# Performance work log

Hardware: AMD Instinct MI355X
Metric: run time of the kernel (lower is better)

The kernel has to match this reference:

```python
import jax, jax.numpy as jnp
import numpy as np

L_LAYERS = 6
DIM = 256
HEADS = 8
FFN = 1024
EPS_LN = 1e-3  # keras LayerNormalization default epsilon
EPS_ATT = 1e-6


def sine_pos_encoding(seq_len, d):
    pos = jnp.arange(seq_len, dtype=jnp.float32)[:, None]
    i = jnp.arange(d, dtype=jnp.float32)[None, :]
    rate = jnp.power(1e4, -(2.0 * jnp.floor(i / 2.0)) / d)
    ang = pos * rate
    return jnp.where(jnp.arange(d)[None, :] % 2 == 0, jnp.sin(ang), jnp.cos(ang))


def layer_norm(x, g, b):
    mu = jnp.mean(x, axis=-1, keepdims=True)
    var = jnp.mean(jnp.square(x - mu), axis=-1, keepdims=True)
    return (x - mu) * jax.lax.rsqrt(var + EPS_LN) * g + b


def lin_attn(xq, xk, xv, Wq, bq, Wk, bk, Wv, bv, Wo, bo):
    B, Lq, _ = xq.shape
    Lk = xk.shape[1]
    dh = DIM // HEADS
    q = (xq @ Wq + bq).reshape(B, Lq, HEADS, dh)
    k = (xk @ Wk + bk).reshape(B, Lk, HEADS, dh)
    v = (xv @ Wv + bv).reshape(B, Lk, HEADS, dh)
    # kernel feature map: elu(x) + 1
    Qf = jax.nn.elu(q) + 1.0
    Kf = jax.nn.elu(k) + 1.0
    KV = jnp.einsum('bshd,bshm->bhdm', Kf, v)            # [B,H,dh,dh]
    Z = 1.0 / (jnp.einsum('blhd,bhd->blh', Qf, Kf.sum(1)) + EPS_ATT)
    out = jnp.einsum('blhd,bhdm,blh->blhm', Qf, KV, Z)   # [B,Lq,H,dh]
    return out.reshape(B, Lq, DIM) @ Wo + bo


def setup_inputs() -> dict:
    key = jax.random.key(0)
    ks = jax.random.split(key, 32)
    s = 0.02
    d = {
        'Q': jax.random.normal(ks[0], (8, 4096, 256), jnp.float32),
        'K': jax.random.normal(ks[1], (8, 4096, 256), jnp.float32),
    }
    def W(k, shape):
        return jax.random.normal(k, shape, jnp.float32) * s
    for sfx, base in (('1', 2), ('2', 10)):
        d['Wq' + sfx] = W(ks[base + 0], (L_LAYERS, DIM, DIM))
        d['Wk' + sfx] = W(ks[base + 1], (L_LAYERS, DIM, DIM))
        d['Wv' + sfx] = W(ks[base + 2], (L_LAYERS, DIM, DIM))
        d['Wo' + sfx] = W(ks[base + 3], (L_LAYERS, DIM, DIM))
        d['bq' + sfx] = jnp.zeros((L_LAYERS, DIM))
        d['bk' + sfx] = jnp.zeros((L_LAYERS, DIM))
        d['bv' + sfx] = jnp.zeros((L_LAYERS, DIM))
        d['bo' + sfx] = jnp.zeros((L_LAYERS, DIM))
    d['Wf1'] = W(ks[20], (L_LAYERS, DIM, FFN))
    d['bf1'] = jnp.zeros((L_LAYERS, FFN))
    d['Wf2'] = W(ks[21], (L_LAYERS, FFN, DIM))
    d['bf2'] = jnp.zeros((L_LAYERS, DIM))
    for nm in ('ln1', 'ln2', 'ln3'):
        d[nm + '_g'] = jnp.ones((L_LAYERS, DIM))
        d[nm + '_b'] = jnp.zeros((L_LAYERS, DIM))
    return d


def reference(Q, K,
              Wq1, Wk1, Wv1, Wo1, bq1, bk1, bv1, bo1,
              Wq2, Wk2, Wv2, Wo2, bq2, bk2, bv2, bo2,
              Wf1, bf1, Wf2, bf2,
              ln1_g, ln1_b, ln2_g, ln2_b, ln3_g, ln3_b):
    pe = sine_pos_encoding(Q.shape[1], Q.shape[2])
    x1 = Q + pe[None]
    for i in range(L_LAYERS):
        x = lin_attn(x1, x1, x1, Wq1[i], bq1[i], Wk1[i], bk1[i], Wv1[i], bv1[i], Wo1[i], bo1[i])
        x2 = layer_norm(x + x1, ln1_g[i], ln1_b[i])
        x = lin_attn(x2, K, K, Wq2[i], bq2[i], Wk2[i], bk2[i], Wv2[i], bv2[i], Wo2[i], bo2[i])
        x3 = layer_norm(x + x2, ln2_g[i], ln2_b[i])
        h = jax.nn.relu(x3 @ Wf1[i] + bf1[i])
        f = jax.nn.relu(h @ Wf2[i] + bf2[i])  # second Dense also has relu
        x1 = layer_norm(f + x3, ln3_g[i], ln3_b[i])
    return x1
```

## Files before the change

### kernel.cpp

```cpp
#include <hip/hip_runtime.h>

#define BATCH 8
#define SEQ 4096
#define DIM 256
#define NH 8
#define DH 32
#define FFN_DIM 1024
#define NL 6
#define M_TOTAL (BATCH * SEQ)
#define NCHUNK 8

typedef __attribute__((ext_vector_type(8))) short s16x8;
typedef __attribute__((ext_vector_type(4))) short s16x4;
typedef __attribute__((ext_vector_type(4))) float f32x4;

__device__ __forceinline__ float bf2f(short s) {
    union { unsigned u; float f; } x;
    x.u = ((unsigned)(unsigned short)s) << 16;
    return x.f;
}
__device__ __forceinline__ short f2bf(float f) {
    union { float f; unsigned u; } x;
    x.f = f;
    unsigned r = x.u + 0x7fffu + ((x.u >> 16) & 1u);
    return (short)(r >> 16);
}

#define GLDS16(gp, sp) __builtin_amdgcn_global_load_lds( \
    (const __attribute__((address_space(1))) void*)(gp), \
    (__attribute__((address_space(3))) void*)(sp), 16, 0, 0)

__global__ void peadd_kernel(const float* __restrict__ Q, short* __restrict__ xb,
                             float* __restrict__ xf, int total)
{
    const float c = 9.210340371976184f / 256.f;
    for (int idx = blockIdx.x * 256 + threadIdx.x; idx < total; idx += gridDim.x * 256) {
        int d = idx & (DIM - 1);
        int l = (idx >> 8) & (SEQ - 1);
        float rate = __expf(-(float)(d & ~1) * c);
        float ang = (float)l * rate;
        float pe = (d & 1) ? cosf(ang) : sinf(ang);
        float v = Q[idx] + pe;
        xb[idx] = f2bf(v);
        xf[idx] = v;
    }
}

__global__ void kconv_kernel(const float* __restrict__ src, short* __restrict__ dst, int total)
{
    for (int idx = blockIdx.x * 256 + threadIdx.x; idx < total; idx += gridDim.x * 256)
        dst[idx] = f2bf(src[idx]);
}

__global__ void wtrans_kernel(const float* __restrict__ W, short* __restrict__ Wt,
                              int K, int N, int lstride, int rowoff)
{
    __shared__ float tile[32][33];
    int k0 = blockIdx.x * 32, n0 = blockIdx.y * 32;
    const float* Wl = W + (long)blockIdx.z * K * N;
    short* Wtl = Wt + (long)blockIdx.z * lstride;
    int tx = threadIdx.x, ty = threadIdx.y;
#pragma unroll
    for (int r = 0; r < 4; ++r)
        tile[ty + r * 8][tx] = Wl[(long)(k0 + ty + r * 8) * N + n0 + tx];
    __syncthreads();
#pragma unroll
    for (int r = 0; r < 4; ++r)
        Wtl[(long)(rowoff + n0 + ty + r * 8) * K + k0 + tx] = f2bf(tile[tx][ty + r * 8]);
}

__global__ void bpack_kernel(const float* __restrict__ bk1, const float* __restrict__ bv1,
                             const float* __restrict__ bk2, const float* __restrict__ bv2,
                             float* __restrict__ o1, float* __restrict__ o2)
{
    int z = blockIdx.x, t = threadIdx.x;
    o1[z * 512 + t] = (t < 256) ? bk1[z * 256 + t] : bv1[z * 256 + t - 256];
    o2[z * 512 + t] = (t < 256) ? bk2[z * 256 + t] : bv2[z * 256 + t - 256];
}

template<int ACT>
__global__ __launch_bounds__(256, 2) void gemm_bt_kernel(
    const short* __restrict__ A, const short* __restrict__ Bt,
    const float* __restrict__ bias, short* __restrict__ Cb,
    int N, int K, int lda, int ldc, int eluCut)
{
    __shared__ short As[2][128][64];
    __shared__ short Bs[2][128][64];
    const int tid = threadIdx.x;
    const int lane = tid & 63;
    const int wid = tid >> 6;
    const int wr = wid >> 1, wc = wid & 1;
    const int bm = blockIdx.x * 128, bn = blockIdx.y * 128;
    const int l15 = lane & 15, l4 = lane >> 4;
    const int rl = lane >> 3;
    const int ch = lane & 7;
    const int nt = K >> 6;

    auto STAGE = [&](int buf, int t) {
        const int k0 = t << 6;
#pragma unroll
        for (int j = 0; j < 8; ++j) {
            int s = wid * 8 + j;
            if (s < 16) {
                int r = s * 8 + rl;
                int cs = ch ^ (r & 7);
                GLDS16(A + (long)(bm + r) * lda + k0 + cs * 8, &As[buf][s * 8][0]);
            } else {
                int r = (s - 16) * 8 + rl;
                int cs = ch ^ (r & 7);
                GLDS16(Bt + (long)(bn + r) * K + k0 + cs * 8, &Bs[buf][(s - 16) * 8][0]);
            }
        }
    };

    f32x4 acc[4][4] = {};

    STAGE(0, 0);
    STAGE(1, 1);
    for (int t = 0; t < nt; ++t) {
        const int buf = t & 1;
        if (t + 1 < nt) { asm volatile("s_waitcnt vmcnt(8)" ::: "memory"); }
        else            { asm volatile("s_waitcnt vmcnt(0)" ::: "memory"); }
        asm volatile("s_barrier" ::: "memory");
        s16x8 avA[2][4], avB[2][4];
        const int sw = l15 & 7;
#pragma unroll
        for (int kk = 0; kk < 2; ++kk) {
#pragma unroll
            for (int m = 0; m < 4; ++m)
                avA[kk][m] = *(const s16x8*)&As[buf][wr * 64 + m * 16 + l15][(((kk << 2) | l4) ^ sw) << 3];
#pragma unroll
            for (int n = 0; n < 4; ++n)
                avB[kk][n] = *(const s16x8*)&Bs[buf][wc * 64 + n * 16 + l15][(((kk << 2) | l4) ^ sw) << 3];
        }
        asm volatile("s_waitcnt lgkmcnt(0)" ::: "memory");
        asm volatile("s_barrier" ::: "memory");
        if (t + 2 < nt) STAGE(buf, t + 2);
#pragma unroll
        for (int kk = 0; kk < 2; ++kk)
#pragma unroll
            for (int m = 0; m < 4; ++m)
#pragma unroll
                for (int n = 0; n < 4; ++n)
                    acc[m][n] = __builtin_amdgcn_mfma_f32_16x16x32_bf16(avA[kk][m], avB[kk][n], acc[m][n], 0, 0, 0);
    }

#pragma unroll
    for (int m = 0; m < 4; ++m) {
        int row0 = bm + wr * 64 + m * 16 + l4 * 4;
#pragma unroll
        for (int n = 0; n < 4; ++n) {
            int col = bn + wc * 64 + n * 16 + l15;
            float bv = bias[col];
#pragma unroll
            for (int j = 0; j < 4; ++j) {
                float v = acc[m][n][j] + bv;
                if (ACT == 1) { if (col < eluCut) v = (v > 0.f) ? v + 1.f : __expf(v); }
                else if (ACT == 2) v = fmaxf(v, 0.f);
                Cb[(long)(row0 + j) * ldc + col] = f2bf(v);
            }
        }
    }
}

__global__ __launch_bounds__(512, 1) void ffnln_kernel(
    const short* __restrict__ X, const short* __restrict__ W1t,
    const float* __restrict__ b1, const short* __restrict__ W2t,
    const float* __restrict__ b2,
    const float* __restrict__ gam, const float* __restrict__ bet,
    const float* __restrict__ Fin, float* __restrict__ Fout,
    short* __restrict__ xb)
{
    __shared__ short xs[4][64][64];
    __shared__ short hs[4][64][64];
    __shared__ short Bs[8][2][32][64];
    __shared__ float partS[8][64];
    __shared__ float partQ[8][64];
    __shared__ float muA[64];
    __shared__ float rsA[64];
    const int tid = threadIdx.x;
    const int lane = tid & 63;
    const int w = tid >> 6;
    const int bm = blockIdx.x * 64;
    const int l15 = lane & 15, l4 = lane >> 4;
    const int rl = lane >> 3;
    const int ch = lane & 7;
    const int sw = l15 & 7;

#pragma unroll
    for (int j = 0; j < 4; ++j) {
        int s = w * 4 + j;
        int kt = s >> 3, rg = s & 7;
        int r = rg * 8 + rl;
        int cs = ch ^ (r & 7);
        GLDS16(X + (long)(bm + r) * 256 + kt * 64 + cs * 8, &xs[kt][rg * 8][0]);
    }
    auto STAGEB = [&](int buf, int v) {
        int hc = v >> 3, u = v & 7;
#pragma unroll
        for (int j = 0; j < 4; ++j) {
            int lr = j * 8 + rl;
            int r = w * 32 + lr;
            int cs = ch ^ (lr & 7);
            const short* src = (u < 4)
                ? W1t + (long)(hc * 256 + r) * 256 + u * 64 + cs * 8
                : W2t + (long)r * 1024 + hc * 256 + (u - 4) * 64 + cs * 8;
            GLDS16(src, &Bs[w][buf][j * 8][0]);
        }
    };

    STAGEB(0, 0);
    STAGEB(1, 1);
    asm volatile("s_waitcnt vmcnt(8)" ::: "memory");
    asm volatile("s_barrier" ::: "memory");

    f32x4 facc[4][2] = {};

    for (int hc = 0; hc < 4; ++hc) {
        f32x4 hacc[4][2] = {};
#pragma unroll
        for (int u = 0; u < 4; ++u) {
            const int v = hc * 8 + u;
            const int buf = v & 1;
            asm volatile("s_waitcnt vmcnt(4)" ::: "memory");
            s16x8 avA[2][4], avB[2][2];
#pragma unroll
            for (int kk = 0; kk < 2; ++kk) {
#pragma unroll
                for (int n = 0; n < 2; ++n)
                    avB[kk][n] = *(const s16x8*)&Bs[w][buf][n * 16 + l15][(((kk << 2) | l4) ^ sw) << 3];
#pragma unroll
                for (int m = 0; m < 4; ++m)
                    avA[kk][m] = *(const s16x8*)&xs[u][m * 16 + l15][(((kk << 2) | l4) ^ sw) << 3];
            }
            asm volatile("s_waitcnt lgkmcnt(0)" ::: "memory");
            STAGEB(buf, v + 2);
#pragma unroll
            for (int kk = 0; kk < 2; ++kk)
#pragma unroll
                for (int m = 0; m < 4; ++m)
#pragma unroll
                    for (int n = 0; n < 2; ++n)
                        hacc[m][n] = __builtin_amdgcn_mfma_f32_16x16x32_bf16(avA[kk][m], avB[kk][n], hacc[m][n], 0, 0, 0);
        }
        asm volatile("s_waitcnt lgkmcnt(0)" ::: "memory");
        asm volatile("s_barrier" ::: "memory");
#pragma unroll
        for (int m = 0; m < 4; ++m)
#pragma unroll
            for (int n = 0; n < 2; ++n) {
                int c = w * 32 + n * 16 + l15;
                float bv = b1[hc * 256 + c];
#pragma unroll
                for (int j = 0; j < 4; ++j) {
                    int r = m * 16 + l4 * 4 + j;
                    float hv = fmaxf(hacc[m][n][j] + bv, 0.f);
                    int kt = c >> 6, cc = (c & 63) >> 3;
                    hs[kt][r][((cc ^ (r & 7)) << 3) + (c & 7)] = f2bf(hv);
                }
            }
        asm volatile("s_waitcnt lgkmcnt(0)" ::: "memory");
        asm volatile("s_barrier" ::: "memory");
#pragma unroll
        for (int u = 4; u < 8; ++u) {
            const int v = hc * 8 + u;
            const int buf = v & 1;
            if (v < 31) { asm volatile("s_waitcnt vmcnt(4)" ::: "memory"); }
            else        { asm volatile("s_waitcnt vmcnt(0)" ::: "memory"); }
            s16x8 avA[2][4], avB[2][2];
#pragma unroll
            for (int kk = 0; kk < 2; ++kk) {
#pragma unroll
                for (int n = 0; n < 2; ++n)
                    avB[kk][n] = *(const s16x8*)&Bs[w][buf][n * 16 + l15][(((kk << 2) | l4) ^ sw) << 3];
#pragma unroll
                for (int m = 0; m < 4; ++m)
                    avA[kk][m] = *(const s16x8*)&hs[u - 4][m * 16 + l15][(((kk << 2) | l4) ^ sw) << 3];
            }
            asm volatile("s_waitcnt lgkmcnt(0)" ::: "memory");
            if (v + 2 < 32) STAGEB(buf, v + 2);
#pragma unroll
            for (int kk = 0; kk < 2; ++kk)
#pragma unroll
                for (int m = 0; m < 4; ++m)
#pragma unroll
                    for (int n = 0; n < 2; ++n)
                        facc[m][n] = __builtin_amdgcn_mfma_f32_16x16x32_bf16(avA[kk][m], avB[kk][n], facc[m][n], 0, 0, 0);
        }
    }

#pragma unroll
    for (int m = 0; m < 4; ++m)
#pragma unroll
        for (int n = 0; n < 2; ++n) {
            int col = w * 32 + n * 16 + l15;
            float bv = b2[col];
#pragma unroll
            for (int j = 0; j < 4; ++j) {
                int r = m * 16 + l4 * 4 + j;
                float v = fmaxf(facc[m][n][j] + bv, 0.f);
                v += Fin[(long)(bm + r) * DIM + col];
                facc[m][n][j] = v;
            }
        }
#pragma unroll
    for (int m = 0; m < 4; ++m)
#pragma unroll
        for (int j = 0; j < 4; ++j) {
            float s = facc[m][0][j] + facc[m][1][j];
            float q = facc[m][0][j] * facc[m][0][j] + facc[m][1][j] * facc[m][1][j];
#pragma unroll
            for (int off = 1; off < 16; off <<= 1) {
                s += __shfl_xor(s, off);
                q += __shfl_xor(q, off);
            }
            if (l15 == 0) {
                partS[w][m * 16 + l4 * 4 + j] = s;
                partQ[w][m * 16 + l4 * 4 + j] = q;
            }
        }
    __syncthreads();
    if (tid < 64) {
        float S = 0, Qq = 0;
#pragma unroll
        for (int ww = 0; ww < 8; ++ww) { S += partS[ww][tid]; Qq += partQ[ww][tid]; }
        float mu = S * (1.f / 256.f);
        float var = Qq * (1.f / 256.f) - mu * mu;
        muA[tid] = mu;
        rsA[tid] = rsqrtf(var + 1e-3f);
    }
    __syncthreads();
#pragma unroll
    for (int m = 0; m < 4; ++m)
#pragma unroll
        for (int j = 0; j < 4; ++j) {
            int r = m * 16 + l4 * 4 + j;
            float mu = muA[r], rs = rsA[r];
#pragma unroll
            for (int n = 0; n < 2; ++n) {
                int col = w * 32 + n * 16 + l15;
                float t = (facc[m][n][j] - mu) * rs * gam[col] + bet[col];
                long o = (long)(bm + r) * DIM + col;
                xb[o] = f2bf(t);
                Fout[o] = t;
            }
        }
}

__global__ __launch_bounds__(512, 1) void qattn_kernel(
    const short* __restrict__ A, const short* __restrict__ Bt,
    const float* __restrict__ bias, const float* __restrict__ kv,
    const float* __restrict__ ksum,
    const short* __restrict__ WoT, const float* __restrict__ bo,
    const float* __restrict__ gam, const float* __restrict__ bet,
    const float* __restrict__ Fin, float* __restrict__ Fout,
    short* __restrict__ xb)
{
    __shared__ char smem[140288];
    short (*As)[128][64] = (short(*)[128][64])(smem);
    short (*Bs)[256][64] = (short(*)[256][64])(smem + 32768);
    short (*QfL)[256] = (short(*)[256])(smem);
    short (*kvbT)[32][48] = (short(*)[32][48])(smem + 98304);
    float* ksumAll = (float*)(smem + 122880);
    float (*partDenH)[128] = (float(*)[128])(smem + 123904);
    short (*oL)[256] = (short(*)[256])(smem + 65536);
    short (*WoS)[256][64] = (short(*)[256][64])(smem);
    float (*partS)[128] = (float(*)[128])(smem + 131072);
    float (*partQ)[128] = (float(*)[128])(smem + 135168);
    float* muA = (float*)(smem + 139264);
    float* rsA = (float*)(smem + 139776);

    const int tid = threadIdx.x;
    const int lane = tid & 63;
    const int w = tid >> 6;
    const int wr = w >> 2, wc = w & 3;
    const int bm = blockIdx.x * 128;
    const int b = bm >> 12;
    const int l15 = lane & 15, l4 = lane >> 4;
    const int rl = lane >> 3;
    const int ch = lane & 7;
    const int sw = l15 & 7;

    for (int idx = tid; idx < 8192; idx += 512) {
        int h = idx >> 10, j = idx & 1023, d = j >> 5, m = j & 31;
        kvbT[h][m][d] = f2bf(kv[(long)(b * 8 + h) * 1024 + j]);
    }
    if (tid < 256) ksumAll[tid] = ksum[(b * 8 + (tid >> 5)) * 32 + (tid & 31)];

    auto STAGE = [&](int buf, int t) {
        const int k0 = t << 6;
#pragma unroll
        for (int j = 0; j < 6; ++j) {
            int s = w * 6 + j;
            if (s < 16) {
                int r = s * 8 + rl;
                int cs = ch ^ (r & 7);
                GLDS16(A + (long)(bm + r) * 256 + k0 + cs * 8, &As[buf][s * 8][0]);
            } else {
                int r = (s - 16) * 8 + rl;
                int cs = ch ^ (r & 7);
                GLDS16(Bt + (long)r * 256 + k0 + cs * 8, &Bs[buf][(s - 16) * 8][0]);
            }
        }
    };

    f32x4 acc[4][4] = {};

    STAGE(0, 0);
    STAGE(1, 1);
#pragma unroll
    for (int t = 0; t < 4; ++t) {
        const int buf = t & 1;
        if (t < 3) { asm volatile("s_waitcnt vmcnt(6)" ::: "memory"); }
        else       { asm volatile("s_waitcnt vmcnt(0)" ::: "memory"); }
        asm volatile("s_barrier" ::: "memory");
        s16x8 avA[2][4], avB[2][4];
#pragma unroll
        for (int kk = 0; kk < 2; ++kk) {
#pragma unroll
            for (int m = 0; m < 4; ++m)
                avA[kk][m] = *(const s16x8*)&As[buf][wr * 64 + m * 16 + l15][(((kk << 2) | l4) ^ sw) << 3];
#pragma unroll
            for (int n = 0; n < 4; ++n)
                avB[kk][n] = *(const s16x8*)&Bs[buf][wc * 64 + n * 16 + l15][(((kk << 2) | l4) ^ sw) << 3];
        }
        asm volatile("s_waitcnt lgkmcnt(0)" ::: "memory");
        asm volatile("s_barrier" ::: "memory");
        if (t < 2) STAGE(buf, t + 2);
#pragma unroll
        for (int kk = 0; kk < 2; ++kk)
#pragma unroll
            for (int m = 0; m < 4; ++m)
#pragma unroll
                for (int n = 0; n < 4; ++n)
                    acc[m][n] = __builtin_amdgcn_mfma_f32_16x16x32_bf16(avA[kk][m], avB[kk][n], acc[m][n], 0, 0, 0);
    }

#pragma unroll
    for (int m = 0; m < 4; ++m)
#pragma unroll
        for (int n = 0; n < 4; ++n) {
            int col = wc * 64 + n * 16 + l15;
            float bv = bias[col];
#pragma unroll
            for (int j = 0; j < 4; ++j) {
                float v = acc[m][n][j] + bv;
                acc[m][n][j] = (v > 0.f) ? v + 1.f : __expf(v);
            }
        }
#pragma unroll
    for (int m = 0; m < 4; ++m)
#pragma unroll
        for (int j = 0; j < 4; ++j) {
            float p0 = acc[m][0][j] * ksumAll[wc * 64 + l15]
                     + acc[m][1][j] * ksumAll[wc * 64 + 16 + l15];
            float p1 = acc[m][2][j] * ksumAll[wc * 64 + 32 + l15]
                     + acc[m][3][j] * ksumAll[wc * 64 + 48 + l15];
#pragma unroll
            for (int off = 1; off < 16; off <<= 1) {
                p0 += __shfl_xor(p0, off);
                p1 += __shfl_xor(p1, off);
            }
            if (l15 == 0) {
                int r = wr * 64 + m * 16 + l4 * 4 + j;
                partDenH[wc * 2 + 0][r] = p0;
                partDenH[wc * 2 + 1][r] = p1;
            }
        }
#pragma unroll
    for (int m = 0; m < 4; ++m)
#pragma unroll
        for (int n = 0; n < 4; ++n) {
            int col = wc * 64 + n * 16 + l15;
#pragma unroll
            for (int j = 0; j < 4; ++j) {
                int r = wr * 64 + m * 16 + l4 * 4 + j;
                int chunk = (col >> 3) ^ (r & 7);
                QfL[r][chunk * 8 + (col & 7)] = f2bf(acc[m][n][j]);
            }
        }
    __syncthreads();

    const int h = w;
    s16x8 afr[2];
#pragma unroll
    for (int ct = 0; ct < 2; ++ct)
        afr[ct] = *(const s16x8*)&kvbT[h][ct * 16 + l15][l4 * 8];
    float zv[8];
#pragma unroll
    for (int rt = 0; rt < 8; ++rt)
        zv[rt] = 1.f / (partDenH[h][rt * 16 + l15] + 1e-6f);
    asm volatile("s_waitcnt lgkmcnt(0)" ::: "memory");
    __syncthreads();

#pragma unroll
    for (int rt = 0; rt < 8; ++rt) {
        int r = rt * 16 + l15;
        int qchunk = (h * 4 + l4) ^ (r & 7);
        s16x8 bfr = *(const s16x8*)&QfL[r][qchunk * 8];
#pragma unroll
        for (int ct = 0; ct < 2; ++ct) {
            f32x4 zero = {0.f, 0.f, 0.f, 0.f};
            f32x4 po = __builtin_amdgcn_mfma_f32_16x16x32_bf16(afr[ct], bfr, zero, 0, 0, 0);
            s16x4 o4;
#pragma unroll
            for (int j = 0; j < 4; ++j) o4[j] = f2bf(po[j] * zv[rt]);
            int c0 = h * 32 + ct * 16 + l4 * 4;
            int cc = c0 >> 3;
            *(s16x4*)&oL[r][((cc ^ (r & 7)) << 3) + (c0 & 7)] = o4;
        }
    }
    asm volatile("s_waitcnt lgkmcnt(0)" ::: "memory");
    __syncthreads();

    auto STAGEWO = [&](int buf, int t) {
#pragma unroll
        for (int j = 0; j < 4; ++j) {
            int lr = j * 8 + rl;
            int r = w * 32 + lr;
            int cs = ch ^ (lr & 7);
            GLDS16(WoT + (long)r * 256 + t * 64 + cs * 8, &WoS[buf][w * 32 + j * 8][0]);
        }
    };
    STAGEWO(0, 0);
    STAGEWO(1, 1);

    f32x4 facc[8][2] = {};
#pragma unroll
    for (int t = 0; t < 4; ++t) {
        const int buf = t & 1;
        if (t < 3) { asm volatile("s_waitcnt vmcnt(4)" ::: "memory"); }
        else       { asm volatile("s_waitcnt vmcnt(0)" ::: "memory"); }
#pragma unroll
        for (int kk = 0; kk < 2; ++kk) {
            s16x8 avB0 = *(const s16x8*)&WoS[buf][w * 32 + l15][(((kk << 2) | l4) ^ sw) << 3];
            s16x8 avB1 = *(const s16x8*)&WoS[buf][w * 32 + 16 + l15][(((kk << 2) | l4) ^ sw) << 3];
#pragma unroll
            for (int m = 0; m < 8; ++m) {
                int ar = m * 16 + l15;
                s16x8 avA = *(const s16x8*)&oL[ar][(t * 8 + (((kk << 2) | l4) ^ sw)) << 3];
                facc[m][0] = __builtin_amdgcn_mfma_f32_16x16x32_bf16(avA, avB0, facc[m][0], 0, 0, 0);
                facc[m][1] = __builtin_amdgcn_mfma_f32_16x16x32_bf16(avA, avB1, facc[m][1], 0, 0, 0);
            }
        }
        asm volatile("s_waitcnt lgkmcnt(0)" ::: "memory");
        if (t + 2 < 4) STAGEWO(buf, t + 2);
    }

#pragma unroll
    for (int m = 0; m < 8; ++m)
#pragma unroll
        for (int n = 0; n < 2; ++n) {
            int col = w * 32 + n * 16 + l15;
            float bv = bo[col];
#pragma unroll
            for (int j = 0; j < 4; ++j) {
                int r = m * 16 + l4 * 4 + j;
                float v = facc[m][n][j] + bv;
                v += Fin[(long)(bm + r) * DIM + col];
                facc[m][n][j] = v;
            }
        }
#pragma unroll
    for (int m = 0; m < 8; ++m)
#pragma unroll
        for (int j = 0; j < 4; ++j) {
            float s = facc[m][0][j] + facc[m][1][j];
            float q = facc[m][0][j] * facc[m][0][j] + facc[m][1][j] * facc[m][1][j];
#pragma unroll
            for (int off = 1; off < 16; off <<= 1) {
                s += __shfl_xor(s, off);
                q += __shfl_xor(q, off);
            }
            if (l15 == 0) {
                partS[w][m * 16 + l4 * 4 + j] = s;
                partQ[w][m * 16 + l4 * 4 + j] = q;
            }
        }
    __syncthreads();
    if (tid < 128) {
        float S = 0, Qq = 0;
#pragma unroll
        for (int ww = 0; ww < 8; ++ww) { S += partS[ww][tid]; Qq += partQ[ww][tid]; }
        float mu = S * (1.f / 256.f);
        float var = Qq * (1.f / 256.f) - mu * mu;
        muA[tid] = mu;
        rsA[tid] = rsqrtf(var + 1e-3f);
    }
    __syncthreads();
#pragma unroll
    for (int m = 0; m < 8; ++m)
#pragma unroll
        for (int j = 0; j < 4; ++j) {
            int r = m * 16 + l4 * 4 + j;
            float mu = muA[r], rs = rsA[r];
#pragma unroll
            for (int n = 0; n < 2; ++n) {
                int col = w * 32 + n * 16 + l15;
                float t = (facc[m][n][j] - mu) * rs * gam[col] + bet[col];
                long o = (long)(bm + r) * DIM + col;
                xb[o] = f2bf(t);
                Fout[o] = t;
            }
        }
}

__global__ __launch_bounds__(256) void kvpart_kernel(
    const short* __restrict__ KV, float* __restrict__ part)
{
    __shared__ float kfs[32][32];
    __shared__ float vsh[32][32];
    int c = blockIdx.x, bh = blockIdx.y;
    int b = bh >> 3, h = bh & 7;
    int tid = threadIdx.x;
    int d = tid >> 3, m0 = (tid & 7) * 4;
    float acc0 = 0, acc1 = 0, acc2 = 0, acc3 = 0, ks = 0;
    long rowBase = ((long)b * SEQ + c * 512) * 512 + h * DH;
    int lrow = (tid & 127) >> 2, cg = tid & 3;
    for (int s0 = 0; s0 < 512; s0 += 32) {
        long rb = rowBase + (long)(s0 + lrow) * 512 + cg * 8 + ((tid < 128) ? 0 : 256);
        s16x8 v8 = *(const s16x8*)(KV + rb);
        float* dst = (tid < 128) ? &kfs[lrow][cg * 8] : &vsh[lrow][cg * 8];
#pragma unroll
        for (int e = 0; e < 8; ++e) dst[e] = bf2f(v8[e]);
        __syncthreads();
#pragma unroll
        for (int s = 0; s < 32; ++s) {
            float kd = kfs[s][d];
            acc0 += kd * vsh[s][m0];
            acc1 += kd * vsh[s][m0 + 1];
            acc2 += kd * vsh[s][m0 + 2];
            acc3 += kd * vsh[s][m0 + 3];
        }
        if (tid < 32) {
#pragma unroll
            for (int s = 0; s < 32; ++s) ks += kfs[s][tid];
        }
        __syncthreads();
    }
    float* pb = part + ((long)bh * NCHUNK + c) * 1056;
    pb[tid * 4 + 0] = acc0; pb[tid * 4 + 1] = acc1;
    pb[tid * 4 + 2] = acc2; pb[tid * 4 + 3] = acc3;
    if (tid < 32) pb[1024 + tid] = ks;
}

__global__ __launch_bounds__(256) void kvred_kernel(
    const float* __restrict__ part, float* __restrict__ kv, float* __restrict__ ksum)
{
    int bh = blockIdx.x, tid = threadIdx.x;
    const float* pb = part + (long)bh * NCHUNK * 1056;
    float s0 = 0, s1 = 0, s2 = 0, s3 = 0;
    for (int cc = 0; cc < NCHUNK; ++cc) {
        const float* p = pb + cc * 1056 + tid * 4;
        s0 += p[0]; s1 += p[1]; s2 += p[2]; s3 += p[3];
    }
    float* kb = kv + (long)bh * 1024 + tid * 4;
    kb[0] = s0; kb[1] = s1; kb[2] = s2; kb[3] = s3;
    if (tid < 32) {
        float ss = 0;
        for (int cc = 0; cc < NCHUNK; ++cc) ss += pb[cc * 1056 + 1024 + tid];
        ksum[bh * 32 + tid] = ss;
    }
}

extern "C" void kernel_launch(void* const* d_in, const int* in_sizes, int n_in,
                              void* d_out, int out_size, void* d_ws, size_t ws_size,
                              hipStream_t stream)
{
    const float* Qin = (const float*)d_in[0];
    const float* Kin = (const float*)d_in[1];
    const float* Wq1 = (const float*)d_in[2];
    const float* Wk1 = (const float*)d_in[3];
    const float* Wv1 = (const float*)d_in[4];
    const float* Wo1 = (const float*)d_in[5];
    const float* bq1 = (const float*)d_in[6];
    const float* bk1 = (const float*)d_in[7];
    const float* bv1 = (const float*)d_in[8];
    const float* bo1 = (const float*)d_in[9];
    const float* Wq2 = (const float*)d_in[10];
    const float* Wk2 = (const float*)d_in[11];
    const float* Wv2 = (const float*)d_in[12];
    const float* Wo2 = (const float*)d_in[13];
    const float* bq2 = (const float*)d_in[14];
    const float* bk2 = (const float*)d_in[15];
    const float* bv2 = (const float*)d_in[16];
    const float* bo2 = (const float*)d_in[17];
    const float* Wf1 = (const float*)d_in[18];
    const float* bf1 = (const float*)d_in[19];
    const float* Wf2 = (const float*)d_in[20];
    const float* bf2 = (const float*)d_in[21];
    const float* ln1g = (const float*)d_in[22];
    const float* ln1b = (const float*)d_in[23];
    const float* ln2g = (const float*)d_in[24];
    const float* ln2b = (const float*)d_in[25];
    const float* ln3g = (const float*)d_in[26];
    const float* ln3b = (const float*)d_in[27];
    (void)in_sizes; (void)n_in; (void)out_size;

    const size_t NEED = 117841920ULL;
    if (ws_size < NEED) return;

    char* ws = (char*)d_ws;
    size_t off = 0;
    auto alloc = [&](size_t bytes) -> void* {
        void* p = ws + off;
        off = (off + bytes + 255) & ~(size_t)255;
        return p;
    };
    const size_t ACT_E = (size_t)M_TOTAL * DIM;

    short* wkv1t = (short*)alloc((size_t)NL * 512 * 256 * 2);
    short* wkv2t = (short*)alloc((size_t)NL * 512 * 256 * 2);
    short* wq1t  = (short*)alloc((size_t)NL * 65536 * 2);
    short* wo1t  = (short*)alloc((size_t)NL * 65536 * 2);
    short* wq2t  = (short*)alloc((size_t)NL * 65536 * 2);
    short* wo2t  = (short*)alloc((size_t)NL * 65536 * 2);
    short* wf1t  = (short*)alloc((size_t)NL * 262144 * 2);
    short* wf2t  = (short*)alloc((size_t)NL * 262144 * 2);
    float* bkv1  = (float*)alloc((size_t)NL * 512 * 4);
    float* bkv2  = (float*)alloc((size_t)NL * 512 * 4);
    short* kbf = (short*)alloc(ACT_E * 2);
    short* A0  = (short*)alloc(ACT_E * 2);
    short* BIG = (short*)alloc((size_t)M_TOTAL * 512 * 2);
    float* Fx  = (float*)alloc(ACT_E * 4);
    float* part = (float*)alloc((size_t)64 * NCHUNK * 1056 * 4);
    float* kvb  = (float*)alloc((size_t)64 * 1024 * 4);
    float* ksb  = (float*)alloc((size_t)64 * 32 * 4);

    peadd_kernel<<<2048, 256, 0, stream>>>(Qin, A0, Fx, (int)ACT_E);
    kconv_kernel<<<2048, 256, 0, stream>>>(Kin, kbf, (int)ACT_E);
    wtrans_kernel<<<dim3(8, 8, NL), dim3(32, 8), 0, stream>>>(Wk1, wkv1t, 256, 256, 512 * 256, 0);
    wtrans_kernel<<<dim3(8, 8, NL), dim3(32, 8), 0, stream>>>(Wv1, wkv1t, 256, 256, 512 * 256, 256);
    wtrans_kernel<<<dim3(8, 8, NL), dim3(32, 8), 0, stream>>>(Wk2, wkv2t, 256, 256, 512 * 256, 0);
    wtrans_kernel<<<dim3(8, 8, NL), dim3(32, 8), 0, stream>>>(Wv2, wkv2t, 256, 256, 512 * 256, 256);
    wtrans_kernel<<<dim3(8, 8, NL), dim3(32, 8), 0, stream>>>(Wq1, wq1t, 256, 256, 65536, 0);
    wtrans_kernel<<<dim3(8, 8, NL), dim3(32, 8), 0, stream>>>(Wo1, wo1t, 256, 256, 65536, 0);
    wtrans_kernel<<<dim3(8, 8, NL), dim3(32, 8), 0, stream>>>(Wq2, wq2t, 256, 256, 65536, 0);
    wtrans_kernel<<<dim3(8, 8, NL), dim3(32, 8), 0, stream>>>(Wo2, wo2t, 256, 256, 65536, 0);
    wtrans_kernel<<<dim3(8, 32, NL), dim3(32, 8), 0, stream>>>(Wf1, wf1t, 256, 1024, 262144, 0);
    wtrans_kernel<<<dim3(32, 8, NL), dim3(32, 8), 0, stream>>>(Wf2, wf2t, 1024, 256, 262144, 0);
    bpack_kernel<<<NL, 512, 0, stream>>>(bk1, bv1, bk2, bv2, bkv1, bkv2);

    dim3 blk(256), blk512(512);

    for (int i = 0; i < NL; ++i) {
        const short* wkv1i = wkv1t + (size_t)i * 512 * 256;
        const short* wkv2i = wkv2t + (size_t)i * 512 * 256;
        const short* wq1i = wq1t + (size_t)i * 65536;
        const short* wo1i = wo1t + (size_t)i * 65536;
        const short* wq2i = wq2t + (size_t)i * 65536;
        const short* wo2i = wo2t + (size_t)i * 65536;
        const short* wf1i = wf1t + (size_t)i * 262144;
        const short* wf2i = wf2t + (size_t)i * 262144;

        gemm_bt_kernel<1><<<dim3(256, 4), blk, 0, stream>>>(A0, wkv1i, bkv1 + i * 512, BIG, 512, 256, 256, 512, 256);
        kvpart_kernel<<<dim3(NCHUNK, 64), blk, 0, stream>>>(BIG, part);
        kvred_kernel<<<64, blk, 0, stream>>>(part, kvb, ksb);
        qattn_kernel<<<M_TOTAL / 128, blk512, 0, stream>>>(A0, wq1i, bq1 + i * 256, kvb, ksb,
            wo1i, bo1 + i * 256, ln1g + i * 256, ln1b + i * 256, Fx, Fx, A0);

        gemm_bt_kernel<1><<<dim3(256, 4), blk, 0, stream>>>(kbf, wkv2i, bkv2 + i * 512, BIG, 512, 256, 256, 512, 256);
        kvpart_kernel<<<dim3(NCHUNK, 64), blk, 0, stream>>>(BIG, part);
        kvred_kernel<<<64, blk, 0, stream>>>(part, kvb, ksb);
        qattn_kernel<<<M_TOTAL / 128, blk512, 0, stream>>>(A0, wq2i, bq2 + i * 256, kvb, ksb,
            wo2i, bo2 + i * 256, ln2g + i * 256, ln2b + i * 256, Fx, Fx, A0);

        ffnln_kernel<<<M_TOTAL / 64, blk512, 0, stream>>>(A0, wf1i, bf1 + i * 1024,
            wf2i, bf2 + i * 256, ln3g + i * 256, ln3b + i * 256,
            Fx, (i == NL - 1) ? (float*)d_out : Fx, A0);
    }
}
```

Measured before the change: 1.357 ms.

## Halve FFN row tile to 32 and narrow weight stages for more occupancy

The fused FFN+LayerNorm kernel now handles 32 rows per block instead of 64. Weight tiles are staged at K=32 granularity with a new swizzle, and launch bounds ask for 4 blocks per CU. The smaller tile cuts LDS and register use so several blocks can share a CU and hide latency. In exchange each weight byte is reused by half as many rows, so weight traffic from L2 doubles and each K-step does fewer MFMAs per barrier or wait.

```diff
diff --git a/kernel.cpp b/kernel.cpp
--- a/kernel.cpp
+++ b/kernel.cpp
@@ -163,7 +163,7 @@
     }
 }
 
-__global__ __launch_bounds__(512, 1) void ffnln_kernel(
+__global__ __launch_bounds__(512, 4) void ffnln_kernel(
     const short* __restrict__ X, const short* __restrict__ W1t,
     const float* __restrict__ b1, const short* __restrict__ W2t,
     const float* __restrict__ b2,
@@ -171,82 +171,83 @@
     const float* __restrict__ Fin, float* __restrict__ Fout,
     short* __restrict__ xb)
 {
-    __shared__ short xs[4][64][64];
-    __shared__ short hs[4][64][64];
-    __shared__ short Bs[8][2][32][64];
-    __shared__ float partS[8][64];
-    __shared__ float partQ[8][64];
-    __shared__ float muA[64];
-    __shared__ float rsA[64];
+    __shared__ short xs[4][32][64];
+    __shared__ short hs[4][32][64];
+    __shared__ short Bs[8][2][32][32];
+    __shared__ float partS[8][32];
+    __shared__ float partQ[8][32];
+    __shared__ float muA[32];
+    __shared__ float rsA[32];
     const int tid = threadIdx.x;
     const int lane = tid & 63;
     const int w = tid >> 6;
-    const int bm = blockIdx.x * 64;
+    const int bm = blockIdx.x * 32;
     const int l15 = lane & 15, l4 = lane >> 4;
     const int rl = lane >> 3;
     const int ch = lane & 7;
     const int sw = l15 & 7;
-
-#pragma unroll
-    for (int j = 0; j < 4; ++j) {
-        int s = w * 4 + j;
-        int kt = s >> 3, rg = s & 7;
+    const int brl = lane >> 2;
+    const int bch = lane & 3;
+
+#pragma unroll
+    for (int j = 0; j < 2; ++j) {
+        int s = w * 2 + j;
+        int kt = s >> 2, rg = s & 3;
         int r = rg * 8 + rl;
         int cs = ch ^ (r & 7);
         GLDS16(X + (long)(bm + r) * 256 + kt * 64 + cs * 8, &xs[kt][rg * 8][0]);
     }
     auto STAGEB = [&](int buf, int v) {
-        int hc = v >> 3, u = v & 7;
-#pragma unroll
-        for (int j = 0; j < 4; ++j) {
-            int lr = j * 8 + rl;
+        int hc = v >> 4, u = v & 15;
+#pragma unroll
+        for (int j = 0; j < 2; ++j) {
+            int lr = j * 16 + brl;
             int r = w * 32 + lr;
-            int cs = ch ^ (lr & 7);
-            const short* src = (u < 4)
-                ? W1t + (long)(hc * 256 + r) * 256 + u * 64 + cs * 8
-                : W2t + (long)r * 1024 + hc * 256 + (u - 4) * 64 + cs * 8;
-            GLDS16(src, &Bs[w][buf][j * 8][0]);
+            int cs = bch ^ ((lr >> 1) & 3);
+            const short* src = (u < 8)
+                ? W1t + (long)(hc * 256 + r) * 256 + u * 32 + cs * 8
+                : W2t + (long)r * 1024 + hc * 256 + (u - 8) * 32 + cs * 8;
+            GLDS16(src, &Bs[w][buf][j * 16][0]);
         }
     };
 
     STAGEB(0, 0);
     STAGEB(1, 1);
-    asm volatile("s_waitcnt vmcnt(8)" ::: "memory");
+    asm volatile("s_waitcnt vmcnt(4)" ::: "memory");
     asm volatile("s_barrier" ::: "memory");
 
-    f32x4 facc[4][2] = {};
+    f32x4 facc[2][2] = {};
 
     for (int hc = 0; hc < 4; ++hc) {
-        f32x4 hacc[4][2] = {};
-#pragma unroll
-        for (int u = 0; u < 4; ++u) {
-            const int v = hc * 8 + u;
+        f32x4 hacc[2][2] = {};
+#pragma unroll
+        for (int u = 0; u < 8; ++u) {
+            const int v = hc * 16 + u;
             const int buf = v & 1;
-            asm volatile("s_waitcnt vmcnt(4)" ::: "memory");
-            s16x8 avA[2][4], avB[2][2];
-#pragma unroll
-            for (int kk = 0; kk < 2; ++kk) {
-#pragma unroll
-                for (int n = 0; n < 2; ++n)
-                    avB[kk][n] = *(const s16x8*)&Bs[w][buf][n * 16 + l15][(((kk << 2) | l4) ^ sw) << 3];
-#pragma unroll
-                for (int m = 0; m < 4; ++m)
-                    avA[kk][m] = *(const s16x8*)&xs[u][m * 16 + l15][(((kk << 2) | l4) ^ sw) << 3];
+            asm volatile("s_waitcnt vmcnt(2)" ::: "memory");
+            s16x8 avA[2], avB[2];
+#pragma unroll
+            for (int n = 0; n < 2; ++n) {
+                int r = n * 16 + l15;
+                avB[n] = *(const s16x8*)&Bs[w][buf][r][(l4 ^ ((r >> 1) & 3)) << 3];
+            }
+#pragma unroll
+            for (int m = 0; m < 2; ++m) {
+                int r = m * 16 + l15;
+                avA[m] = *(const s16x8*)&xs[u >> 1][r][((((u & 1) << 2) | l4) ^ sw) << 3];
             }
             asm volatile("s_waitcnt lgkmcnt(0)" ::: "memory");
             STAGEB(buf, v + 2);
 #pragma unroll
-            for (int kk = 0; kk < 2; ++kk)
-#pragma unroll
-                for (int m = 0; m < 4; ++m)
-#pragma unroll
-                    for (int n = 0; n < 2; ++n)
-                        hacc[m][n] = __builtin_amdgcn_mfma_f32_16x16x32_bf16(avA[kk][m], avB[kk][n], hacc[m][n], 0, 0, 0);
+            for (int m = 0; m < 2; ++m)
+#pragma unroll
+                for (int n = 0; n < 2; ++n)
+                    hacc[m][n] = __builtin_amdgcn_mfma_f32_16x16x32_bf16(avA[m], avB[n], hacc[m][n], 0, 0, 0);
         }
         asm volatile("s_waitcnt lgkmcnt(0)" ::: "memory");
         asm volatile("s_barrier" ::: "memory");
 #pragma unroll
-        for (int m = 0; m < 4; ++m)
+        for (int m = 0; m < 2; ++m)
 #pragma unroll
             for (int n = 0; n < 2; ++n) {
                 int c = w * 32 + n * 16 + l15;
@@ -262,35 +263,35 @@
         asm volatile("s_waitcnt lgkmcnt(0)" ::: "memory");
         asm volatile("s_barrier" ::: "memory");
 #pragma unroll
-        for (int u = 4; u < 8; ++u) {
-            const int v = hc * 8 + u;
+        for (int u = 8; u < 16; ++u) {
+            const int v = hc * 16 + u;
             const int buf = v & 1;
-            if (v < 31) { asm volatile("s_waitcnt vmcnt(4)" ::: "memory"); }
+            if (v < 62) { asm volatile("s_waitcnt vmcnt(2)" ::: "memory"); }
             else        { asm volatile("s_waitcnt vmcnt(0)" ::: "memory"); }
-            s16x8 avA[2][4], avB[2][2];
-#pragma unroll
-            for (int kk = 0; kk < 2; ++kk) {
+            s16x8 avA[2], avB[2];
+#pragma unroll
+            for (int n = 0; n < 2; ++n) {
+                int r = n * 16 + l15;
+                avB[n] = *(const s16x8*)&Bs[w][buf][r][(l4 ^ ((r >> 1) & 3)) << 3];
+            }
+            int uu = u - 8;
+#pragma unroll
+            for (int m = 0; m < 2; ++m) {
+                int r = m * 16 + l15;
+                avA[m] = *(const s16x8*)&hs[uu >> 1][r][((((uu & 1) << 2) | l4) ^ sw) << 3];
+            }
+            asm volatile("s_waitcnt lgkmcnt(0)" ::: "memory");
+            if (v + 2 < 64) STAGEB(buf, v + 2);
+#pragma unroll
+            for (int m = 0; m < 2; ++m)
 #pragma unroll
                 for (int n = 0; n < 2; ++n)
-                    avB[kk][n] = *(const s16x8*)&Bs[w][buf][n * 16 + l15][(((kk << 2) | l4) ^ sw) << 3];
-#pragma unroll
-                for (int m = 0; m < 4; ++m)
-                    avA[kk][m] = *(const s16x8*)&hs[u - 4][m * 16 + l15][(((kk << 2) | l4) ^ sw) << 3];
-            }
-            asm volatile("s_waitcnt lgkmcnt(0)" ::: "memory");
-            if (v + 2 < 32) STAGEB(buf, v + 2);
-#pragma unroll
-            for (int kk = 0; kk < 2; ++kk)
-#pragma unroll
-                for (int m = 0; m < 4; ++m)
-#pragma unroll
-                    for (int n = 0; n < 2; ++n)
-                        facc[m][n] = __builtin_amdgcn_mfma_f32_16x16x32_bf16(avA[kk][m], avB[kk][n], facc[m][n], 0, 0, 0);
-        }
-    }
-
-#pragma unroll
-    for (int m = 0; m < 4; ++m)
+                    facc[m][n] = __builtin_amdgcn_mfma_f32_16x16x32_bf16(avA[m], avB[n], facc[m][n], 0, 0, 0);
+        }
+    }
+
+#pragma unroll
+    for (int m = 0; m < 2; ++m)
 #pragma unroll
         for (int n = 0; n < 2; ++n) {
             int col = w * 32 + n * 16 + l15;
@@ -304,7 +305,7 @@
             }
         }
 #pragma unroll
-    for (int m = 0; m < 4; ++m)
+    for (int m = 0; m < 2; ++m)
 #pragma unroll
         for (int j = 0; j < 4; ++j) {
             float s = facc[m][0][j] + facc[m][1][j];
@@ -320,7 +321,7 @@
             }
         }
     __syncthreads();
-    if (tid < 64) {
+    if (tid < 32) {
         float S = 0, Qq = 0;
 #pragma unroll
         for (int ww = 0; ww < 8; ++ww) { S += partS[ww][tid]; Qq += partQ[ww][tid]; }
@@ -331,7 +332,7 @@
     }
     __syncthreads();
 #pragma unroll
-    for (int m = 0; m < 4; ++m)
+    for (int m = 0; m < 2; ++m)
 #pragma unroll
         for (int j = 0; j < 4; ++j) {
             int r = m * 16 + l4 * 4 + j;
@@ -765,7 +766,7 @@
         qattn_kernel<<<M_TOTAL / 128, blk512, 0, stream>>>(A0, wq2i, bq2 + i * 256, kvb, ksb,
             wo2i, bo2 + i * 256, ln2g + i * 256, ln2b + i * 256, Fx, Fx, A0);
 
-        ffnln_kernel<<<M_TOTAL / 64, blk512, 0, stream>>>(A0, wf1i, bf1 + i * 1024,
+        ffnln_kernel<<<M_TOTAL / 32, blk512, 0, stream>>>(A0, wf1i, bf1 + i * 1024,
             wf2i, bf2 + i * 256, ln3g + i * 256, ln3b + i * 256,
             Fx, (i == NL - 1) ? (float*)d_out : Fx, A0);
     }
```

Result: slower. 1.439 ms (+6.0%).
